# Kernel tuning notes

Hardware: AMD Instinct MI355X
Metric: run time of the kernel (lower is better)

Reference implementation:

```python
import jax, jax.numpy as jnp
import numpy as np

B, N, Z, E, K = 2, 64, 128, 64, 64


def setup_inputs() -> dict:
    key = jax.random.key(0)
    ks = jax.random.split(key, 8)
    emb1 = jax.random.normal(ks[0], (B, N, Z), dtype=jnp.float32)
    ef = jax.random.normal(ks[1], (B, N, N, E), dtype=jnp.float32)
    Wz = jax.random.normal(ks[2], (3, Z, K), dtype=jnp.float32) / np.float32(np.sqrt(Z))
    bz = jnp.zeros((3, K), dtype=jnp.float32)
    Wef = jax.random.normal(ks[3], (3, E, K), dtype=jnp.float32) / np.float32(np.sqrt(E))
    # pattern embedding: 6 rows, padding_idx=0 -> row 0 is zeros
    table = jax.random.normal(ks[4], (6, K), dtype=jnp.float32).at[0].set(0.0)
    Wm = jax.random.normal(ks[5], (2, K, K), dtype=jnp.float32) / np.float32(np.sqrt(K))
    bm = jnp.zeros((2, K), dtype=jnp.float32)
    return {"emb1": emb1, "ef": ef, "Wz": Wz, "bz": bz, "Wef": Wef,
            "table": table, "Wm": Wm, "bm": bm}


def _tuple_pattern(n):
    # start at 1, diag(i,i,i)=2, (i,:,i)=3, (:,j,j)=4, (i,i,:)=5
    idx = jnp.arange(n)
    tp = jnp.ones((n, n, n), dtype=jnp.int32)
    tp = tp.at[idx, idx, idx].set(2)
    tp = tp.at[idx, :, idx].set(3)
    tp = tp.at[:, idx, idx].set(4)
    tp = tp.at[idx, idx, :].set(5)
    return tp


def reference(emb1, ef, Wz, bz, Wef, table, Wm, bm):
    # z_lins: Dense(Z->K) with SiLU activation
    z0 = jax.nn.silu(emb1 @ Wz[0] + bz[0])  # (B,N,K)
    z1 = jax.nn.silu(emb1 @ Wz[1] + bz[1])
    z2 = jax.nn.silu(emb1 @ Wz[2] + bz[2])
    # ef_lins: Dense(E->K), no bias, no activation
    e0 = ef @ Wef[0]  # (B,N,N,K)
    e1 = ef @ Wef[1]
    e2 = ef @ Wef[2]
    # 3-way outer broadcasts -> (B,N,N,N,K)
    z_mixed = z0[:, None, None, :, :] * z1[:, :, None, None, :] * z2[:, None, :, None, :]
    ef_mixed = e0[:, None, :, :, :] * e1[:, :, None, :, :] * e2[:, :, :, None, :]
    n = emb1.shape[1]
    pat = table[_tuple_pattern(n)]  # (N,N,N,K)
    x = z_mixed * ef_mixed * pat[None]  # (B,N,N,N,K)
    # Residual(mlp_num=2): two Dense(K->K, SiLU) layers + skip
    h = jax.nn.silu(x @ Wm[0] + bm[0])
    h = jax.nn.silu(h @ Wm[1] + bm[1])
    return h + x
```

## Files before the change

kernel.cpp:

```cpp
#include <hip/hip_runtime.h>

typedef __attribute__((ext_vector_type(4))) float f4;
typedef __attribute__((ext_vector_type(8))) short bf8;
typedef __attribute__((ext_vector_type(4))) float f32x4;
typedef __attribute__((ext_vector_type(2))) unsigned int u32x2;
typedef __attribute__((ext_vector_type(4))) unsigned int u32x4;

__device__ __forceinline__ float silu_f(float v) {
    return v * __builtin_amdgcn_rcpf(1.0f + __expf(-v));
}
__device__ __forceinline__ ushort f2bf(float f) {
    unsigned u = __float_as_uint(f);
    u += 0x7fff + ((u >> 16) & 1);
    return (ushort)(u >> 16);
}
__device__ __forceinline__ unsigned cvtpk(float lo, float hi) {
    unsigned r;
    asm("v_cvt_pk_bf16_f32 %0, %1, %2" : "=v"(r) : "v"(lo), "v"(hi));
    return r;
}
__device__ __forceinline__ void cvt8(u32x4 v, f4& lo, f4& hi) {
    lo[0] = __uint_as_float(v[0] << 16);
    lo[1] = __uint_as_float(v[0] & 0xffff0000u);
    lo[2] = __uint_as_float(v[1] << 16);
    lo[3] = __uint_as_float(v[1] & 0xffff0000u);
    hi[0] = __uint_as_float(v[2] << 16);
    hi[1] = __uint_as_float(v[2] & 0xffff0000u);
    hi[2] = __uint_as_float(v[3] << 16);
    hi[3] = __uint_as_float(v[3] & 0xffff0000u);
}

extern "C" __global__ void k_zw(const float* __restrict__ emb1,
                                const float* __restrict__ Wz,
                                const float* __restrict__ bz,
                                const float* __restrict__ Wm,
                                float* __restrict__ z,
                                ushort* __restrict__ WT) {
    if (blockIdx.x < 96) {
        int tid = blockIdx.x * 256 + threadIdx.x;
        int k = tid & 63;
        int n = (tid >> 6) & 63;
        int b = (tid >> 12) & 1;
        int l = tid >> 13;
        const float* er = emb1 + (b * 64 + n) * 128;
        const float* w  = Wz + l * 8192 + k;
        float acc = bz[l * 64 + k];
        #pragma unroll 8
        for (int c = 0; c < 128; ++c) acc = fmaf(er[c], w[c * 64], acc);
        z[tid] = silu_f(acc);
    } else {
        int tid = (blockIdx.x - 96) * 256 + threadIdx.x;
        int l = tid >> 12, n = (tid >> 6) & 63, k = tid & 63;
        WT[tid] = f2bf(Wm[l * 4096 + k * 64 + n]);
    }
}

extern "C" __global__ void k_e(const float* __restrict__ ef,
                               const float* __restrict__ Wef,
                               const float* __restrict__ z,
                               ushort* __restrict__ e) {
    int tid = blockIdx.x * 256 + threadIdx.x;
    int k0  = (tid & 15) * 4;
    int row = (tid >> 4) & 8191;
    int l   = tid >> 17;
    const float* efr = ef + row * 64;
    const float* w   = Wef + l * 4096 + k0;
    f4 acc = {0.f, 0.f, 0.f, 0.f};
    #pragma unroll
    for (int c4 = 0; c4 < 16; ++c4) {
        f4 ev = *(const f4*)(efr + c4 * 4);
        #pragma unroll
        for (int q = 0; q < 4; ++q)
            acc += ev[q] * *(const f4*)(w + (c4 * 4 + q) * 64);
    }
    int b  = row >> 12;
    int mn = (l == 1) ? ((row >> 6) & 63) : (row & 63);
    acc *= *(const f4*)(z + l * 8192 + b * 4096 + mn * 64 + k0);
    u32x2 pk = {cvtpk(acc[0], acc[1]), cvtpk(acc[2], acc[3])};
    *(u32x2*)(e + l * 524288 + row * 64 + k0) = pk;
}

extern "C" __global__ void __launch_bounds__(256, 4)
k_main(const ushort* __restrict__ e, const float* __restrict__ table,
       const ushort* __restrict__ WT, const float* __restrict__ bm,
       float* __restrict__ out) {
    __shared__ ushort Wl[8192];
    __shared__ ushort XH[8192];

    const int t   = threadIdx.x;
    const int bid = blockIdx.x;
    const int jq = bid & 15;
    const int i  = (bid >> 4) & 63;
    const int b  = bid >> 10;
    const int j0 = jq * 4;

    #pragma unroll
    for (int p = 0; p < 4; ++p) {
        int g   = p * 256 + t;
        int row = g >> 3;
        int cb  = (g & 7) * 16;
        u32x4 v = *(const u32x4*)(WT + g * 8);
        *(u32x4*)((char*)Wl + row * 128 + (cb ^ ((row & 7) << 4))) = v;
    }

    const int r  = t >> 2;
    const int c0 = (t & 3) << 4;
    const int ln = t & 63, w = t >> 6;
    const int lr = ln & 15, lg = ln >> 4;
    const int abyte = (w * 16 + lr) * 128;
    const int arx   = (lr & 7) << 4;
    const int orr = ln >> 3, os = ln & 7;
    const int obrow = ((lr & 8) ? (8192 + w * 2048) : (w * 2048)) + (lr & 7) * 256;

    const ushort* e1p = e + 524288 + ((b * 64 + i) * 64 + r) * 64 + c0;
    u32x4 e1r0 = *(const u32x4*)(e1p);
    u32x4 e1r1 = *(const u32x4*)(e1p + 8);
    f4 pe1t[4];
    {
        f4 a, bq, c, d;
        cvt8(e1r0, a, bq); cvt8(e1r1, c, d);
        pe1t[0] = a  * *(const f4*)(table + 64 + c0);
        pe1t[1] = bq * *(const f4*)(table + 64 + c0 + 4);
        pe1t[2] = c  * *(const f4*)(table + 64 + c0 + 8);
        pe1t[3] = d  * *(const f4*)(table + 64 + c0 + 12);
    }

    const ushort* e0base = e + ((b * 64 + j0) * 64 + r) * 64 + c0;
    const ushort* e2base = e + 1048576 + ((b * 64 + i) * 64 + j0) * 64 + c0;
    float* ob = out + (size_t)((b * 64 + i) * 64 + j0) * 4096;

    u32x4 ce0a = *(const u32x4*)(e0base);
    u32x4 ce0b = *(const u32x4*)(e0base + 8);

    __syncthreads();

    #pragma unroll 1
    for (int jt = 0; jt < 4; ++jt) {
        const int jj = j0 + jt;

        {
            const ushort* e2p = e2base + jt * 64;
            u32x4 e2a = *(const u32x4*)(e2p);
            u32x4 e2b = *(const u32x4*)(e2p + 8);
            f4 e0f[4], e2f[4];
            cvt8(ce0a, e0f[0], e0f[1]); cvt8(ce0b, e0f[2], e0f[3]);
            cvt8(e2a,  e2f[0], e2f[1]); cvt8(e2b,  e2f[2], e2f[3]);
            f4 xv[4];
            bool slow = (i == jj) || (r == jj) || (r == i);
            if (slow) {
                int p = (i == jj) ? 5 : (jj == r) ? 4 : 3;
                const float* pp = table + p * 64 + c0;
                f4 e1f[4];
                cvt8(e1r0, e1f[0], e1f[1]); cvt8(e1r1, e1f[2], e1f[3]);
                #pragma unroll
                for (int q = 0; q < 4; ++q)
                    xv[q] = e1f[q] * *(const f4*)(pp + 4 * q) * e2f[q] * e0f[q];
            } else {
                #pragma unroll
                for (int q = 0; q < 4; ++q)
                    xv[q] = pe1t[q] * e2f[q] * e0f[q];
            }
            unsigned xw[8];
            #pragma unroll
            for (int q = 0; q < 4; ++q) {
                xw[2 * q]     = cvtpk(xv[q][0], xv[q][1]);
                xw[2 * q + 1] = cvtpk(xv[q][2], xv[q][3]);
            }
            char* rowp = (char*)XH + r * 128;
            const int rx = (r & 7) << 4;
            u32x4 vlo = {xw[0], xw[1], xw[2], xw[3]};
            u32x4 vhi = {xw[4], xw[5], xw[6], xw[7]};
            *(u32x4*)(rowp + ((c0 * 2)      ^ rx)) = vlo;
            *(u32x4*)(rowp + ((c0 * 2 + 16) ^ rx)) = vhi;
        }

        if (jt < 3) {
            const ushort* ne0 = e0base + (jt + 1) * 4096;
            ce0a = *(const u32x4*)(ne0);
            ce0b = *(const u32x4*)(ne0 + 8);
        }

        bf8 a0 = *(const bf8*)((const char*)XH + abyte + ((     lg * 16) ^ arx));
        bf8 a1 = *(const bf8*)((const char*)XH + abyte + ((64 + lg * 16) ^ arx));
        #pragma unroll
        for (int nt = 0; nt < 4; ++nt) {
            const char* wb = (const char*)Wl + (nt * 16 + lr) * 128;
            bf8 b0 = *(const bf8*)(wb + ((     lg * 16) ^ arx));
            bf8 b1 = *(const bf8*)(wb + ((64 + lg * 16) ^ arx));
            f32x4 acc = *(const f4*)(bm + nt * 16 + lg * 4);
            acc = __builtin_amdgcn_mfma_f32_16x16x32_bf16(b0, a0, acc, 0, 0, 0);
            acc = __builtin_amdgcn_mfma_f32_16x16x32_bf16(b1, a1, acc, 0, 0, 0);
            unsigned pk0 = cvtpk(silu_f(acc[0]), silu_f(acc[1]));
            unsigned pk1 = cvtpk(silu_f(acc[2]), silu_f(acc[3]));
            u32x2 hv = {pk0, pk1};
            *(u32x2*)((char*)XH + 8192 + abyte + ((nt * 32 + lg * 8) ^ arx)) = hv;
        }

        bf8 h0 = *(const bf8*)((const char*)XH + 8192 + abyte + ((     lg * 16) ^ arx));
        bf8 h1 = *(const bf8*)((const char*)XH + 8192 + abyte + ((64 + lg * 16) ^ arx));
        u32x2 rrv[4];
        #pragma unroll
        for (int nt = 0; nt < 4; ++nt)
            rrv[nt] = *(const u32x2*)((const char*)XH + abyte +
                                      ((nt * 32 + lg * 8) ^ arx));
        #pragma unroll
        for (int nt = 0; nt < 4; ++nt) {
            const char* wb = (const char*)Wl + (64 + nt * 16 + lr) * 128;
            bf8 b0 = *(const bf8*)(wb + ((     lg * 16) ^ arx));
            bf8 b1 = *(const bf8*)(wb + ((64 + lg * 16) ^ arx));
            f32x4 acc = *(const f4*)(bm + 64 + nt * 16 + lg * 4);
            acc = __builtin_amdgcn_mfma_f32_16x16x32_bf16(b0, h0, acc, 0, 0, 0);
            acc = __builtin_amdgcn_mfma_f32_16x16x32_bf16(b1, h1, acc, 0, 0, 0);
            f4 ov;
            ov[0] = silu_f(acc[0]) + __uint_as_float(rrv[nt][0] << 16);
            ov[1] = silu_f(acc[1]) + __uint_as_float(rrv[nt][0] & 0xffff0000u);
            ov[2] = silu_f(acc[2]) + __uint_as_float(rrv[nt][1] << 16);
            ov[3] = silu_f(acc[3]) + __uint_as_float(rrv[nt][1] & 0xffff0000u);
            *(f4*)((char*)XH + obrow + ((nt * 64 + lg * 16) ^ ((lr & 7) << 4))) = ov;
        }

        float* obj = ob + (size_t)jt * 4096 + w * 16 * 64;
        #pragma unroll
        for (int v = 0; v < 4; ++v) {
            const int rw = (v & 1) * 8 + orr;
            const int rbase = ((v & 1) ? (8192 + w * 2048) : (w * 2048))
                            + (rw & 7) * 256;
            f4 val = *(const f4*)((const char*)XH + rbase +
                     ((((v >> 1) * 128) + os * 16) ^ ((rw & 7) << 4)));
            *(f4*)(obj + rw * 64 + (v >> 1) * 32 + os * 4) = val;
        }
    }
}

extern "C" void kernel_launch(void* const* d_in, const int* in_sizes, int n_in,
                              void* d_out, int out_size, void* d_ws, size_t ws_size,
                              hipStream_t stream) {
    const float* emb1  = (const float*)d_in[0];
    const float* ef    = (const float*)d_in[1];
    const float* Wz    = (const float*)d_in[2];
    const float* bz    = (const float*)d_in[3];
    const float* Wef   = (const float*)d_in[4];
    const float* table = (const float*)d_in[5];
    const float* Wm    = (const float*)d_in[6];
    const float* bm    = (const float*)d_in[7];
    float* out = (float*)d_out;

    float*  zbuf = (float*)d_ws;
    ushort* ebuf = (ushort*)(zbuf + 24576);
    ushort* WT   = ebuf + 1572864;

    k_zw  <<<128,  256, 0, stream>>>(emb1, Wz, bz, Wm, zbuf, WT);
    k_e   <<<1536, 256, 0, stream>>>(ef, Wef, zbuf, ebuf);
    k_main<<<2048, 256, 0, stream>>>(ebuf, table, WT, bm, out);
}
```

Before: 59.75 us.

## Read MLP weights directly from global in MFMA fragment layout, drop LDS staging

The weight transpose kernel now writes Wm into a fragment-ordered layout so that each lane of k_main can load its MFMA B operands straight from global memory (cached in L1/L2), instead of staging the whole weight matrix into LDS. This removes 16KB of LDS per block, the weight staging loop and the __syncthreads barrier, and raises the launch bound to 6 blocks per CU. The e1 row load is moved into the rare slow path, reducing register pressure, and output stores become nontemporal. The cost is repeated global/L2 loads of weights on every jt iteration, which could add latency on the critical path of the MFMAs.

```diff
diff --git a/kernel.cpp b/kernel.cpp
--- a/kernel.cpp
+++ b/kernel.cpp
@@ -35,7 +35,7 @@
                                 const float* __restrict__ bz,
                                 const float* __restrict__ Wm,
                                 float* __restrict__ z,
-                                ushort* __restrict__ WT) {
+                                ushort* __restrict__ FW) {
     if (blockIdx.x < 96) {
         int tid = blockIdx.x * 256 + threadIdx.x;
         int k = tid & 63;
@@ -50,8 +50,15 @@
         z[tid] = silu_f(acc);
     } else {
         int tid = (blockIdx.x - 96) * 256 + threadIdx.x;
-        int l = tid >> 12, n = (tid >> 6) & 63, k = tid & 63;
-        WT[tid] = f2bf(Wm[l * 4096 + k * 64 + n]);
+        int m  = tid & 7;
+        int ln = (tid >> 3) & 63;
+        int h  = (tid >> 9) & 1;
+        int nt = (tid >> 10) & 3;
+        int l  = tid >> 12;
+        int lr = ln & 15, lg = ln >> 4;
+        int k = h * 32 + lg * 8 + m;
+        int n = nt * 16 + lr;
+        FW[tid] = f2bf(Wm[l * 4096 + k * 64 + n]);
     }
 }
 
@@ -80,11 +87,10 @@
     *(u32x2*)(e + l * 524288 + row * 64 + k0) = pk;
 }
 
-extern "C" __global__ void __launch_bounds__(256, 4)
+extern "C" __global__ void __launch_bounds__(256, 6)
 k_main(const ushort* __restrict__ e, const float* __restrict__ table,
-       const ushort* __restrict__ WT, const float* __restrict__ bm,
+       const ushort* __restrict__ FW, const float* __restrict__ bm,
        float* __restrict__ out) {
-    __shared__ ushort Wl[8192];
     __shared__ ushort XH[8192];
 
     const int t   = threadIdx.x;
@@ -93,15 +99,6 @@
     const int i  = (bid >> 4) & 63;
     const int b  = bid >> 10;
     const int j0 = jq * 4;
-
-    #pragma unroll
-    for (int p = 0; p < 4; ++p) {
-        int g   = p * 256 + t;
-        int row = g >> 3;
-        int cb  = (g & 7) * 16;
-        u32x4 v = *(const u32x4*)(WT + g * 8);
-        *(u32x4*)((char*)Wl + row * 128 + (cb ^ ((row & 7) << 4))) = v;
-    }
 
     const int r  = t >> 2;
     const int c0 = (t & 3) << 4;
@@ -111,12 +108,13 @@
     const int arx   = (lr & 7) << 4;
     const int orr = ln >> 3, os = ln & 7;
     const int obrow = ((lr & 8) ? (8192 + w * 2048) : (w * 2048)) + (lr & 7) * 256;
+    const int lnoff = ln * 16;
 
     const ushort* e1p = e + 524288 + ((b * 64 + i) * 64 + r) * 64 + c0;
-    u32x4 e1r0 = *(const u32x4*)(e1p);
-    u32x4 e1r1 = *(const u32x4*)(e1p + 8);
     f4 pe1t[4];
     {
+        u32x4 e1r0 = *(const u32x4*)(e1p);
+        u32x4 e1r1 = *(const u32x4*)(e1p + 8);
         f4 a, bq, c, d;
         cvt8(e1r0, a, bq); cvt8(e1r1, c, d);
         pe1t[0] = a  * *(const f4*)(table + 64 + c0);
@@ -132,11 +130,15 @@
     u32x4 ce0a = *(const u32x4*)(e0base);
     u32x4 ce0b = *(const u32x4*)(e0base + 8);
 
-    __syncthreads();
+    unsigned long long fwa = (unsigned long long)FW;
+    unsigned long long bma = (unsigned long long)bm;
 
     #pragma unroll 1
     for (int jt = 0; jt < 4; ++jt) {
         const int jj = j0 + jt;
+        asm volatile("" : "+s"(fwa), "+s"(bma));
+        const char*  fwt = (const char*)fwa + lnoff;
+        const float* bmt = (const float*)bma;
 
         {
             const ushort* e2p = e2base + jt * 64;
@@ -150,6 +152,8 @@
             if (slow) {
                 int p = (i == jj) ? 5 : (jj == r) ? 4 : 3;
                 const float* pp = table + p * 64 + c0;
+                u32x4 e1r0 = *(const u32x4*)(e1p);
+                u32x4 e1r1 = *(const u32x4*)(e1p + 8);
                 f4 e1f[4];
                 cvt8(e1r0, e1f[0], e1f[1]); cvt8(e1r1, e1f[2], e1f[3]);
                 #pragma unroll
@@ -184,10 +188,9 @@
         bf8 a1 = *(const bf8*)((const char*)XH + abyte + ((64 + lg * 16) ^ arx));
         #pragma unroll
         for (int nt = 0; nt < 4; ++nt) {
-            const char* wb = (const char*)Wl + (nt * 16 + lr) * 128;
-            bf8 b0 = *(const bf8*)(wb + ((     lg * 16) ^ arx));
-            bf8 b1 = *(const bf8*)(wb + ((64 + lg * 16) ^ arx));
-            f32x4 acc = *(const f4*)(bm + nt * 16 + lg * 4);
+            bf8 b0 = *(const bf8*)(fwt + (nt * 2    ) * 1024);
+            bf8 b1 = *(const bf8*)(fwt + (nt * 2 + 1) * 1024);
+            f32x4 acc = *(const f4*)(bmt + nt * 16 + lg * 4);
             acc = __builtin_amdgcn_mfma_f32_16x16x32_bf16(b0, a0, acc, 0, 0, 0);
             acc = __builtin_amdgcn_mfma_f32_16x16x32_bf16(b1, a1, acc, 0, 0, 0);
             unsigned pk0 = cvtpk(silu_f(acc[0]), silu_f(acc[1]));
@@ -205,10 +208,9 @@
                                       ((nt * 32 + lg * 8) ^ arx));
         #pragma unroll
         for (int nt = 0; nt < 4; ++nt) {
-            const char* wb = (const char*)Wl + (64 + nt * 16 + lr) * 128;
-            bf8 b0 = *(const bf8*)(wb + ((     lg * 16) ^ arx));
-            bf8 b1 = *(const bf8*)(wb + ((64 + lg * 16) ^ arx));
-            f32x4 acc = *(const f4*)(bm + 64 + nt * 16 + lg * 4);
+            bf8 b0 = *(const bf8*)(fwt + (8 + nt * 2    ) * 1024);
+            bf8 b1 = *(const bf8*)(fwt + (8 + nt * 2 + 1) * 1024);
+            f32x4 acc = *(const f4*)(bmt + 64 + nt * 16 + lg * 4);
             acc = __builtin_amdgcn_mfma_f32_16x16x32_bf16(b0, h0, acc, 0, 0, 0);
             acc = __builtin_amdgcn_mfma_f32_16x16x32_bf16(b1, h1, acc, 0, 0, 0);
             f4 ov;
@@ -227,7 +229,8 @@
                             + (rw & 7) * 256;
             f4 val = *(const f4*)((const char*)XH + rbase +
                      ((((v >> 1) * 128) + os * 16) ^ ((rw & 7) << 4)));
-            *(f4*)(obj + rw * 64 + (v >> 1) * 32 + os * 4) = val;
+            __builtin_nontemporal_store(val,
+                (f4*)(obj + rw * 64 + (v >> 1) * 32 + os * 4));
         }
     }
 }
@@ -247,9 +250,9 @@
 
     float*  zbuf = (float*)d_ws;
     ushort* ebuf = (ushort*)(zbuf + 24576);
-    ushort* WT   = ebuf + 1572864;
-
-    k_zw  <<<128,  256, 0, stream>>>(emb1, Wz, bz, Wm, zbuf, WT);
+    ushort* FW   = ebuf + 1572864;
+
+    k_zw  <<<128,  256, 0, stream>>>(emb1, Wz, bz, Wm, zbuf, FW);
     k_e   <<<1536, 256, 0, stream>>>(ef, Wef, zbuf, ebuf);
-    k_main<<<2048, 256, 0, stream>>>(ebuf, table, WT, bm, out);
-}
+    k_main<<<2048, 256, 0, stream>>>(ebuf, table, FW, bm, out);
+}
```

Measured after the change: 97.61 us. +63.4%, slower.

## Fuse z projection into edge kernel, remap block order, prefetch e2 rows

Applied to the files above, without the earlier changes.

Removes the separate k_zw launch. Each k_e thread now recomputes its four-wide slice of the SiLU(emb1·Wz) projection inline, and the Wm transpose moves into extra blocks of k_e. k_main remaps block indices so that consecutive hardware blocks spread across groups of i rows, which is meant to change L2 locality on the chiplet layout. It also prefetches the next e2 row during the loop, the same way e0 is already prefetched. The costs are redundant z computation (a 128-long dot product per thread, repeated across 64 rows) and more registers in k_main.

```diff
diff --git a/kernel.cpp b/kernel.cpp
--- a/kernel.cpp
+++ b/kernel.cpp
@@ -30,39 +30,35 @@
     hi[3] = __uint_as_float(v[3] & 0xffff0000u);
 }
 
-extern "C" __global__ void k_zw(const float* __restrict__ emb1,
-                                const float* __restrict__ Wz,
-                                const float* __restrict__ bz,
-                                const float* __restrict__ Wm,
-                                float* __restrict__ z,
-                                ushort* __restrict__ WT) {
-    if (blockIdx.x < 96) {
-        int tid = blockIdx.x * 256 + threadIdx.x;
-        int k = tid & 63;
-        int n = (tid >> 6) & 63;
-        int b = (tid >> 12) & 1;
-        int l = tid >> 13;
-        const float* er = emb1 + (b * 64 + n) * 128;
-        const float* w  = Wz + l * 8192 + k;
-        float acc = bz[l * 64 + k];
-        #pragma unroll 8
-        for (int c = 0; c < 128; ++c) acc = fmaf(er[c], w[c * 64], acc);
-        z[tid] = silu_f(acc);
-    } else {
-        int tid = (blockIdx.x - 96) * 256 + threadIdx.x;
+extern "C" __global__ void k_e(const float* __restrict__ ef,
+                               const float* __restrict__ Wef,
+                               const float* __restrict__ emb1,
+                               const float* __restrict__ Wz,
+                               const float* __restrict__ bz,
+                               const float* __restrict__ Wm,
+                               ushort* __restrict__ e,
+                               ushort* __restrict__ WT) {
+    if (blockIdx.x >= 1536) {
+        int tid = (blockIdx.x - 1536) * 256 + threadIdx.x;
         int l = tid >> 12, n = (tid >> 6) & 63, k = tid & 63;
         WT[tid] = f2bf(Wm[l * 4096 + k * 64 + n]);
-    }
-}
-
-extern "C" __global__ void k_e(const float* __restrict__ ef,
-                               const float* __restrict__ Wef,
-                               const float* __restrict__ z,
-                               ushort* __restrict__ e) {
+        return;
+    }
     int tid = blockIdx.x * 256 + threadIdx.x;
     int k0  = (tid & 15) * 4;
     int row = (tid >> 4) & 8191;
     int l   = tid >> 17;
+    int b   = row >> 12;
+    int mn  = (l == 1) ? ((row >> 6) & 63) : (row & 63);
+
+    const float* er = emb1 + (b * 64 + mn) * 128;
+    const float* wz = Wz + l * 8192 + k0;
+    f4 zv = *(const f4*)(bz + l * 64 + k0);
+    #pragma unroll 8
+    for (int c = 0; c < 128; ++c) zv += er[c] * *(const f4*)(wz + c * 64);
+    #pragma unroll
+    for (int q = 0; q < 4; ++q) zv[q] = silu_f(zv[q]);
+
     const float* efr = ef + row * 64;
     const float* w   = Wef + l * 4096 + k0;
     f4 acc = {0.f, 0.f, 0.f, 0.f};
@@ -73,9 +69,7 @@
         for (int q = 0; q < 4; ++q)
             acc += ev[q] * *(const f4*)(w + (c4 * 4 + q) * 64);
     }
-    int b  = row >> 12;
-    int mn = (l == 1) ? ((row >> 6) & 63) : (row & 63);
-    acc *= *(const f4*)(z + l * 8192 + b * 4096 + mn * 64 + k0);
+    acc *= zv;
     u32x2 pk = {cvtpk(acc[0], acc[1]), cvtpk(acc[2], acc[3])};
     *(u32x2*)(e + l * 524288 + row * 64 + k0) = pk;
 }
@@ -88,11 +82,14 @@
     __shared__ ushort XH[8192];
 
     const int t   = threadIdx.x;
-    const int bid = blockIdx.x;
-    const int jq = bid & 15;
-    const int i  = (bid >> 4) & 63;
-    const int b  = bid >> 10;
-    const int j0 = jq * 4;
+    const int raw = blockIdx.x;
+    const int sem = (raw & 7) * 256 + (raw >> 3);
+    const int ig  = sem >> 8;
+    const int pos = sem & 255;
+    const int b   = pos >> 7;
+    const int jq  = (pos >> 3) & 15;
+    const int i   = ig * 8 + (pos & 7);
+    const int j0  = jq * 4;
 
     #pragma unroll
     for (int p = 0; p < 4; ++p) {
@@ -131,6 +128,8 @@
 
     u32x4 ce0a = *(const u32x4*)(e0base);
     u32x4 ce0b = *(const u32x4*)(e0base + 8);
+    u32x4 ce2a = *(const u32x4*)(e2base);
+    u32x4 ce2b = *(const u32x4*)(e2base + 8);
 
     __syncthreads();
 
@@ -139,12 +138,9 @@
         const int jj = j0 + jt;
 
         {
-            const ushort* e2p = e2base + jt * 64;
-            u32x4 e2a = *(const u32x4*)(e2p);
-            u32x4 e2b = *(const u32x4*)(e2p + 8);
             f4 e0f[4], e2f[4];
             cvt8(ce0a, e0f[0], e0f[1]); cvt8(ce0b, e0f[2], e0f[3]);
-            cvt8(e2a,  e2f[0], e2f[1]); cvt8(e2b,  e2f[2], e2f[3]);
+            cvt8(ce2a, e2f[0], e2f[1]); cvt8(ce2b, e2f[2], e2f[3]);
             f4 xv[4];
             bool slow = (i == jj) || (r == jj) || (r == i);
             if (slow) {
@@ -176,8 +172,11 @@
 
         if (jt < 3) {
             const ushort* ne0 = e0base + (jt + 1) * 4096;
+            const ushort* ne2 = e2base + (jt + 1) * 64;
             ce0a = *(const u32x4*)(ne0);
             ce0b = *(const u32x4*)(ne0 + 8);
+            ce2a = *(const u32x4*)(ne2);
+            ce2b = *(const u32x4*)(ne2 + 8);
         }
 
         bf8 a0 = *(const bf8*)((const char*)XH + abyte + ((     lg * 16) ^ arx));
@@ -245,11 +244,9 @@
     const float* bm    = (const float*)d_in[7];
     float* out = (float*)d_out;
 
-    float*  zbuf = (float*)d_ws;
-    ushort* ebuf = (ushort*)(zbuf + 24576);
+    ushort* ebuf = (ushort*)d_ws;
     ushort* WT   = ebuf + 1572864;
 
-    k_zw  <<<128,  256, 0, stream>>>(emb1, Wz, bz, Wm, zbuf, WT);
-    k_e   <<<1536, 256, 0, stream>>>(ef, Wef, zbuf, ebuf);
+    k_e   <<<1568, 256, 0, stream>>>(ef, Wef, emb1, Wz, bz, Wm, ebuf, WT);
     k_main<<<2048, 256, 0, stream>>>(ebuf, table, WT, bm, out);
 }
```

Measured after the change: 78.49 us. +31.4%, slower.
